# Kernel tuning notes

Measured on AMD Instinct MI355X. Metric: run time of the kernel, lower is better.

## Reference

```python
import jax, jax.numpy as jnp
import numpy as np

I, H = 64, 128


def setup_inputs() -> dict:
    key = jax.random.key(0)
    k1, k2, k3, k4, k5, k6 = jax.random.split(key, 6)
    B, T = 4096, 200
    stdv = 1.0 / np.sqrt(H)
    inp = jax.random.normal(k1, (B, T, I), dtype=jnp.float32)
    seq_lengths = jax.random.randint(k2, (B,), 0, T, dtype=jnp.int32)
    # PyTorch GRUCell params: weight_ih [3H, I], weight_hh [3H, H], biases [3H]; gate order r, z, n
    W_ih = jax.random.uniform(k3, (3 * H, I), minval=-stdv, maxval=stdv, dtype=jnp.float32)
    W_hh = jax.random.uniform(k4, (3 * H, H), minval=-stdv, maxval=stdv, dtype=jnp.float32)
    b_ih = jax.random.uniform(k5, (3 * H,), minval=-stdv, maxval=stdv, dtype=jnp.float32)
    b_hh = jax.random.uniform(k6, (3 * H,), minval=-stdv, maxval=stdv, dtype=jnp.float32)
    return {"input": inp, "seq_lengths": seq_lengths, "W_ih": W_ih, "W_hh": W_hh, "b_ih": b_ih, "b_hh": b_hh}


def _gru_cell(x, h, W_ih, W_hh, b_ih, b_hh):
    gx = x @ W_ih.T + b_ih  # [B, 3H]
    gh = h @ W_hh.T + b_hh  # [B, 3H]
    xr, xz, xn = jnp.split(gx, 3, axis=1)
    hr, hz, hn = jnp.split(gh, 3, axis=1)
    r = jax.nn.sigmoid(xr + hr)
    z = jax.nn.sigmoid(xz + hz)
    n = jnp.tanh(xn + r * hn)
    return (1.0 - z) * n + z * h


def reference(input, seq_lengths, W_ih, W_hh, b_ih, b_hh):
    B, T, _ = input.shape
    h0 = jnp.zeros((B, H), dtype=input.dtype)
    hn0 = jnp.zeros((B, H), dtype=input.dtype)
    xs = (jnp.swapaxes(input, 0, 1), jnp.arange(T))  # [T, B, I], [T]

    def step(carry, xt):
        h, hn = carry
        x_t, t = xt
        h_new = _gru_cell(x_t, h, W_ih, W_hh, b_ih, b_hh)
        mask = (t + 1 <= seq_lengths).astype(input.dtype)[:, None]  # [B, 1]
        hn_new = mask * h_new + (1.0 - mask) * hn
        return (h_new, hn_new), None

    (_, hn_final), _ = jax.lax.scan(step, (h0, hn0), xs)
    return hn_final
```

## Files before the change

### kernel.cpp

```cpp
#include <hip/hip_runtime.h>


#define I_DIM 64
#define H_DIM 128
#define LDSP 200

typedef _Float16 h8 __attribute__((ext_vector_type(8)));
typedef _Float16 h2 __attribute__((ext_vector_type(2)));
typedef float f4 __attribute__((ext_vector_type(4)));
typedef float f2 __attribute__((ext_vector_type(2)));

__device__ __forceinline__ float fast_rcp(float x) {
    return __builtin_amdgcn_rcpf(x);
}
__device__ __forceinline__ float sigmoid_f(float x) {
    return fast_rcp(1.0f + __expf(-x));
}
__device__ __forceinline__ float tanh_f(float x) {
    return 1.0f - 2.0f * fast_rcp(__expf(2.0f * x) + 1.0f);
}

__global__ __launch_bounds__(512, 2)
void gru_seq_kernel(const float* __restrict__ input,
                    const int* __restrict__ seq_lengths,
                    const float* __restrict__ W_ih,
                    const float* __restrict__ W_hh,
                    const float* __restrict__ b_ih,
                    const float* __restrict__ b_hh,
                    float* __restrict__ out,
                    int B, int T) {
    __shared__ __align__(16) _Float16 a_lds[2][16][LDSP];

    const int tid  = threadIdx.x;
    const int lane = tid & 63;
    const int w    = tid >> 6;
    const int base = blockIdx.x * 16;

    const int lrow = lane & 15;
    const int kgrp = lane >> 4;

    int Lq[4];
#pragma unroll
    for (int q = 0; q < 4; ++q) {
        int gr = base + kgrp * 4 + q;
        Lq[q] = (gr < B) ? seq_lengths[gr] : 0;
    }
    int Lmax = 0;
    for (int i = 0; i < 16; ++i) {
        int gr = base + i;
        int L = (gr < B) ? seq_lengths[gr] : 0;
        Lmax = max(Lmax, L);
    }
    if (Lmax > T) Lmax = T;

    const int c0 = w * 16 + lrow;
    const float br  = b_ih[c0] + b_hh[c0];
    const float bz  = b_ih[H_DIM + c0] + b_hh[H_DIM + c0];
    const float bnh = b_hh[2 * H_DIM + c0];
    const float bnx = b_ih[2 * H_DIM + c0];

    h8 bw[18];
#pragma unroll
    for (int gate = 0; gate < 3; ++gate) {
        const int j = gate * H_DIM + w * 16 + lrow;
#pragma unroll
        for (int kt = 0; kt < 6; ++kt) {
            const int kb = kt * 32 + kgrp * 8;
            const float* src = (kt < 4) ? (W_hh + j * H_DIM + kb)
                                        : (W_ih + j * I_DIM + (kb - H_DIM));
            f4 f0 = *(const f4*)(src);
            f4 f1 = *(const f4*)(src + 4);
            h8 v;
            v[0] = (_Float16)f0[0]; v[1] = (_Float16)f0[1];
            v[2] = (_Float16)f0[2]; v[3] = (_Float16)f0[3];
            v[4] = (_Float16)f1[0]; v[5] = (_Float16)f1[1];
            v[6] = (_Float16)f1[2]; v[7] = (_Float16)f1[3];
            bw[gate * 6 + kt] = v;
        }
    }

    {
        int idx = tid * 4;
        int r = idx >> 7, cc = idx & 127;
        *(h2*)&a_lds[0][r][cc]     = h2{0, 0};
        *(h2*)&a_lds[0][r][cc + 2] = h2{0, 0};
    }
    const int xrow = tid >> 5;
    const int xc2  = (tid & 31) * 2;
    const float* xbase = input + (size_t)(base + xrow) * T * I_DIM + xc2;
    const bool xrow_ok = (base + xrow) < B;
    if (Lmax > 0 && xrow_ok) {
        f2 xv = *(const f2*)(xbase);
        h2 hv; hv[0] = (_Float16)xv[0]; hv[1] = (_Float16)xv[1];
        *(h2*)&a_lds[0][xrow][H_DIM + xc2] = hv;
    }
    __syncthreads();

    float hreg[4]  = {0.f, 0.f, 0.f, 0.f};
    float hnreg[4] = {0.f, 0.f, 0.f, 0.f};

    for (int t = 0; t < Lmax; ++t) {
        const int cur = t & 1, nxt = cur ^ 1;

        f2 xn_v = {0.f, 0.f};
        const bool pf = (t + 1 < Lmax) && xrow_ok;
        if (pf) xn_v = *(const f2*)(xbase + (size_t)(t + 1) * I_DIM);

        h8 af[6];
#pragma unroll
        for (int kt = 0; kt < 6; ++kt)
            af[kt] = *(const h8*)&a_lds[cur][lrow][kt * 32 + kgrp * 8];

        f4 ar  = f4{br, br, br, br};
        f4 az  = f4{bz, bz, bz, bz};
        f4 anh = f4{bnh, bnh, bnh, bnh};
        f4 anx = f4{bnx, bnx, bnx, bnx};
#pragma unroll
        for (int kt = 0; kt < 6; ++kt)
            ar = __builtin_amdgcn_mfma_f32_16x16x32_f16(af[kt], bw[0 * 6 + kt], ar, 0, 0, 0);
#pragma unroll
        for (int kt = 0; kt < 6; ++kt)
            az = __builtin_amdgcn_mfma_f32_16x16x32_f16(af[kt], bw[1 * 6 + kt], az, 0, 0, 0);
#pragma unroll
        for (int kt = 0; kt < 4; ++kt)
            anh = __builtin_amdgcn_mfma_f32_16x16x32_f16(af[kt], bw[2 * 6 + kt], anh, 0, 0, 0);
#pragma unroll
        for (int kt = 4; kt < 6; ++kt)
            anx = __builtin_amdgcn_mfma_f32_16x16x32_f16(af[kt], bw[2 * 6 + kt], anx, 0, 0, 0);

#pragma unroll
        for (int q = 0; q < 4; ++q) {
            float r    = sigmoid_f(ar[q]);
            float z    = sigmoid_f(az[q]);
            float n    = tanh_f(anx[q] + r * anh[q]);
            float h    = hreg[q];
            float hnew = n + z * (h - n);
            hreg[q] = hnew;
            if (t < Lq[q]) hnreg[q] = hnew;
        }

#pragma unroll
        for (int q = 0; q < 4; ++q)
            a_lds[nxt][kgrp * 4 + q][w * 16 + lrow] = (_Float16)hreg[q];
        if (pf) {
            h2 hv; hv[0] = (_Float16)xn_v[0]; hv[1] = (_Float16)xn_v[1];
            *(h2*)&a_lds[nxt][xrow][H_DIM + xc2] = hv;
        }
        __syncthreads();
    }

#pragma unroll
    for (int q = 0; q < 4; ++q) {
        int gr = base + kgrp * 4 + q;
        if (gr < B) out[(size_t)gr * H_DIM + w * 16 + lrow] = hnreg[q];
    }
}

extern "C" void kernel_launch(void* const* d_in, const int* in_sizes, int n_in,
                              void* d_out, int out_size, void* d_ws, size_t ws_size,
                              hipStream_t stream) {
    const float* input = (const float*)d_in[0];
    const int*   seq   = (const int*)d_in[1];
    const float* W_ih  = (const float*)d_in[2];
    const float* W_hh  = (const float*)d_in[3];
    const float* b_ih  = (const float*)d_in[4];
    const float* b_hh  = (const float*)d_in[5];
    float* out = (float*)d_out;

    const int B = in_sizes[1];
    const int T = in_sizes[0] / (B * I_DIM);

    const int grid = (B + 15) / 16;
    gru_seq_kernel<<<grid, 512, 0, stream>>>(input, seq, W_ih, W_hh, b_ih, b_hh, out, B, T);
}
```

Measured before the change: 167.5 us.

## Stage input in 8-step chunks and precompute next-step input projection off critical path

```diff
diff --git a/kernel.cpp b/kernel.cpp
--- a/kernel.cpp
+++ b/kernel.cpp
@@ -3,12 +3,13 @@
 
 #define I_DIM 64
 #define H_DIM 128
-#define LDSP 200
+#define CH 8
+#define HP 136
+#define XP 72
 
 typedef _Float16 h8 __attribute__((ext_vector_type(8)));
-typedef _Float16 h2 __attribute__((ext_vector_type(2)));
+typedef _Float16 h4 __attribute__((ext_vector_type(4)));
 typedef float f4 __attribute__((ext_vector_type(4)));
-typedef float f2 __attribute__((ext_vector_type(2)));
 
 __device__ __forceinline__ float fast_rcp(float x) {
     return __builtin_amdgcn_rcpf(x);
@@ -29,7 +30,8 @@
                     const float* __restrict__ b_hh,
                     float* __restrict__ out,
                     int B, int T) {
-    __shared__ __align__(16) _Float16 a_lds[2][16][LDSP];
+    __shared__ __align__(16) _Float16 h_lds[2][16][HP];
+    __shared__ __align__(16) _Float16 x_lds[2][CH][16][XP];
 
     const int tid  = threadIdx.x;
     const int lane = tid & 63;
@@ -62,7 +64,7 @@
     h8 bw[18];
 #pragma unroll
     for (int gate = 0; gate < 3; ++gate) {
-        const int j = gate * H_DIM + w * 16 + lrow;
+        const int j = gate * H_DIM + c0;
 #pragma unroll
         for (int kt = 0; kt < 6; ++kt) {
             const int kb = kt * 32 + kgrp * 8;
@@ -82,19 +84,48 @@
     {
         int idx = tid * 4;
         int r = idx >> 7, cc = idx & 127;
-        *(h2*)&a_lds[0][r][cc]     = h2{0, 0};
-        *(h2*)&a_lds[0][r][cc + 2] = h2{0, 0};
-    }
-    const int xrow = tid >> 5;
-    const int xc2  = (tid & 31) * 2;
-    const float* xbase = input + (size_t)(base + xrow) * T * I_DIM + xc2;
-    const bool xrow_ok = (base + xrow) < B;
-    if (Lmax > 0 && xrow_ok) {
-        f2 xv = *(const f2*)(xbase);
-        h2 hv; hv[0] = (_Float16)xv[0]; hv[1] = (_Float16)xv[1];
-        *(h2*)&a_lds[0][xrow][H_DIM + xc2] = hv;
+        *(h4*)&h_lds[0][r][cc] = h4{0, 0, 0, 0};
+    }
+
+    const int srow = tid >> 5;
+    const int si0  = (tid & 31) >> 4;
+    const int icol = (tid & 15) * 4;
+    const int gxr  = base + srow;
+    const float* xsrc = input + (size_t)gxr * T * I_DIM;
+    const bool xok = (gxr < B);
+
+    if (Lmax > 0) {
+        f4 xv[4];
+#pragma unroll
+        for (int j = 0; j < 4; ++j) {
+            int s = si0 + 2 * j;
+            xv[j] = f4{0.f, 0.f, 0.f, 0.f};
+            if (xok && s < T) xv[j] = *(const f4*)(xsrc + (size_t)s * I_DIM + icol);
+        }
+#pragma unroll
+        for (int j = 0; j < 4; ++j) {
+            int s = si0 + 2 * j;
+            h4 hv;
+            hv[0] = (_Float16)xv[j][0]; hv[1] = (_Float16)xv[j][1];
+            hv[2] = (_Float16)xv[j][2]; hv[3] = (_Float16)xv[j][3];
+            *(h4*)&x_lds[0][s][srow][icol] = hv;
+        }
     }
     __syncthreads();
+
+    f4 arx  = f4{br, br, br, br};
+    f4 azx  = f4{bz, bz, bz, bz};
+    f4 anxx = f4{bnx, bnx, bnx, bnx};
+    if (Lmax > 0) {
+        h8 xg0 = *(const h8*)&x_lds[0][0][lrow][kgrp * 8];
+        h8 xg1 = *(const h8*)&x_lds[0][0][lrow][32 + kgrp * 8];
+        arx  = __builtin_amdgcn_mfma_f32_16x16x32_f16(xg0, bw[0 * 6 + 4], arx, 0, 0, 0);
+        arx  = __builtin_amdgcn_mfma_f32_16x16x32_f16(xg1, bw[0 * 6 + 5], arx, 0, 0, 0);
+        azx  = __builtin_amdgcn_mfma_f32_16x16x32_f16(xg0, bw[1 * 6 + 4], azx, 0, 0, 0);
+        azx  = __builtin_amdgcn_mfma_f32_16x16x32_f16(xg1, bw[1 * 6 + 5], azx, 0, 0, 0);
+        anxx = __builtin_amdgcn_mfma_f32_16x16x32_f16(xg0, bw[2 * 6 + 4], anxx, 0, 0, 0);
+        anxx = __builtin_amdgcn_mfma_f32_16x16x32_f16(xg1, bw[2 * 6 + 5], anxx, 0, 0, 0);
+    }
 
     float hreg[4]  = {0.f, 0.f, 0.f, 0.f};
     float hnreg[4] = {0.f, 0.f, 0.f, 0.f};
@@ -102,37 +133,61 @@
     for (int t = 0; t < Lmax; ++t) {
         const int cur = t & 1, nxt = cur ^ 1;
 
-        f2 xn_v = {0.f, 0.f};
-        const bool pf = (t + 1 < Lmax) && xrow_ok;
-        if (pf) xn_v = *(const f2*)(xbase + (size_t)(t + 1) * I_DIM);
-
-        h8 af[6];
-#pragma unroll
-        for (int kt = 0; kt < 6; ++kt)
-            af[kt] = *(const h8*)&a_lds[cur][lrow][kt * 32 + kgrp * 8];
-
-        f4 ar  = f4{br, br, br, br};
-        f4 az  = f4{bz, bz, bz, bz};
-        f4 anh = f4{bnh, bnh, bnh, bnh};
-        f4 anx = f4{bnx, bnx, bnx, bnx};
-#pragma unroll
-        for (int kt = 0; kt < 6; ++kt)
-            ar = __builtin_amdgcn_mfma_f32_16x16x32_f16(af[kt], bw[0 * 6 + kt], ar, 0, 0, 0);
-#pragma unroll
-        for (int kt = 0; kt < 6; ++kt)
-            az = __builtin_amdgcn_mfma_f32_16x16x32_f16(af[kt], bw[1 * 6 + kt], az, 0, 0, 0);
-#pragma unroll
-        for (int kt = 0; kt < 4; ++kt)
-            anh = __builtin_amdgcn_mfma_f32_16x16x32_f16(af[kt], bw[2 * 6 + kt], anh, 0, 0, 0);
-#pragma unroll
-        for (int kt = 4; kt < 6; ++kt)
-            anx = __builtin_amdgcn_mfma_f32_16x16x32_f16(af[kt], bw[2 * 6 + kt], anx, 0, 0, 0);
+        f4 xv[4];
+        const bool do_stage = ((t & 7) == 0) && (t + CH < Lmax);
+        if (do_stage) {
+            const int t0 = t + CH;
+#pragma unroll
+            for (int j = 0; j < 4; ++j) {
+                int s = si0 + 2 * j;
+                xv[j] = f4{0.f, 0.f, 0.f, 0.f};
+                if (xok && t0 + s < T) xv[j] = *(const f4*)(xsrc + (size_t)(t0 + s) * I_DIM + icol);
+            }
+        }
+
+        h8 af0 = *(const h8*)&h_lds[cur][lrow][0 * 32 + kgrp * 8];
+        h8 af1 = *(const h8*)&h_lds[cur][lrow][1 * 32 + kgrp * 8];
+        h8 af2 = *(const h8*)&h_lds[cur][lrow][2 * 32 + kgrp * 8];
+        h8 af3 = *(const h8*)&h_lds[cur][lrow][3 * 32 + kgrp * 8];
+        const int slot1 = ((t + 1) >> 3) & 1;
+        const int ss1   = (t + 1) & 7;
+        h8 xg0 = *(const h8*)&x_lds[slot1][ss1][lrow][kgrp * 8];
+        h8 xg1 = *(const h8*)&x_lds[slot1][ss1][lrow][32 + kgrp * 8];
+
+        f4 ar   = arx;
+        f4 az   = azx;
+        f4 anxc = anxx;
+        f4 anh  = f4{bnh, bnh, bnh, bnh};
+        __builtin_amdgcn_s_setprio(1);
+        ar  = __builtin_amdgcn_mfma_f32_16x16x32_f16(af0, bw[0 * 6 + 0], ar, 0, 0, 0);
+        ar  = __builtin_amdgcn_mfma_f32_16x16x32_f16(af1, bw[0 * 6 + 1], ar, 0, 0, 0);
+        ar  = __builtin_amdgcn_mfma_f32_16x16x32_f16(af2, bw[0 * 6 + 2], ar, 0, 0, 0);
+        ar  = __builtin_amdgcn_mfma_f32_16x16x32_f16(af3, bw[0 * 6 + 3], ar, 0, 0, 0);
+        az  = __builtin_amdgcn_mfma_f32_16x16x32_f16(af0, bw[1 * 6 + 0], az, 0, 0, 0);
+        az  = __builtin_amdgcn_mfma_f32_16x16x32_f16(af1, bw[1 * 6 + 1], az, 0, 0, 0);
+        az  = __builtin_amdgcn_mfma_f32_16x16x32_f16(af2, bw[1 * 6 + 2], az, 0, 0, 0);
+        az  = __builtin_amdgcn_mfma_f32_16x16x32_f16(af3, bw[1 * 6 + 3], az, 0, 0, 0);
+        anh = __builtin_amdgcn_mfma_f32_16x16x32_f16(af0, bw[2 * 6 + 0], anh, 0, 0, 0);
+        anh = __builtin_amdgcn_mfma_f32_16x16x32_f16(af1, bw[2 * 6 + 1], anh, 0, 0, 0);
+        anh = __builtin_amdgcn_mfma_f32_16x16x32_f16(af2, bw[2 * 6 + 2], anh, 0, 0, 0);
+        anh = __builtin_amdgcn_mfma_f32_16x16x32_f16(af3, bw[2 * 6 + 3], anh, 0, 0, 0);
+        f4 nrx  = f4{br, br, br, br};
+        f4 nzx  = f4{bz, bz, bz, bz};
+        f4 nnx  = f4{bnx, bnx, bnx, bnx};
+        nrx = __builtin_amdgcn_mfma_f32_16x16x32_f16(xg0, bw[0 * 6 + 4], nrx, 0, 0, 0);
+        nrx = __builtin_amdgcn_mfma_f32_16x16x32_f16(xg1, bw[0 * 6 + 5], nrx, 0, 0, 0);
+        nzx = __builtin_amdgcn_mfma_f32_16x16x32_f16(xg0, bw[1 * 6 + 4], nzx, 0, 0, 0);
+        nzx = __builtin_amdgcn_mfma_f32_16x16x32_f16(xg1, bw[1 * 6 + 5], nzx, 0, 0, 0);
+        nnx = __builtin_amdgcn_mfma_f32_16x16x32_f16(xg0, bw[2 * 6 + 4], nnx, 0, 0, 0);
+        nnx = __builtin_amdgcn_mfma_f32_16x16x32_f16(xg1, bw[2 * 6 + 5], nnx, 0, 0, 0);
+        __builtin_amdgcn_s_setprio(0);
+        arx = nrx; azx = nzx; anxx = nnx;
 
 #pragma unroll
         for (int q = 0; q < 4; ++q) {
             float r    = sigmoid_f(ar[q]);
             float z    = sigmoid_f(az[q]);
-            float n    = tanh_f(anx[q] + r * anh[q]);
+            float n    = tanh_f(anxc[q] + r * anh[q]);
             float h    = hreg[q];
             float hnew = n + z * (h - n);
             hreg[q] = hnew;
@@ -141,10 +196,17 @@
 
 #pragma unroll
         for (int q = 0; q < 4; ++q)
-            a_lds[nxt][kgrp * 4 + q][w * 16 + lrow] = (_Float16)hreg[q];
-        if (pf) {
-            h2 hv; hv[0] = (_Float16)xn_v[0]; hv[1] = (_Float16)xn_v[1];
-            *(h2*)&a_lds[nxt][xrow][H_DIM + xc2] = hv;
+            h_lds[nxt][kgrp * 4 + q][c0] = (_Float16)hreg[q];
+        if (do_stage) {
+            const int wslot = ((t >> 3) & 1) ^ 1;
+#pragma unroll
+            for (int j = 0; j < 4; ++j) {
+                int s = si0 + 2 * j;
+                h4 hv;
+                hv[0] = (_Float16)xv[j][0]; hv[1] = (_Float16)xv[j][1];
+                hv[2] = (_Float16)xv[j][2]; hv[3] = (_Float16)xv[j][3];
+                *(h4*)&x_lds[wslot][s][srow][icol] = hv;
+            }
         }
         __syncthreads();
     }
@@ -152,7 +214,7 @@
 #pragma unroll
     for (int q = 0; q < 4; ++q) {
         int gr = base + kgrp * 4 + q;
-        if (gr < B) out[(size_t)gr * H_DIM + w * 16 + lrow] = hnreg[q];
+        if (gr < B) out[(size_t)gr * H_DIM + c0] = hnreg[q];
     }
 }
 
```

New measurement: 158.9 us. 1.05x faster.

## Precompute next-step input projections and stage input chunks across timesteps

Applied to the files above, without the earlier changes.

```diff
diff --git a/kernel.cpp b/kernel.cpp
--- a/kernel.cpp
+++ b/kernel.cpp
@@ -3,22 +3,16 @@
 
 #define I_DIM 64
 #define H_DIM 128
-#define LDSP 200
+#define CH 8
+#define RS 40
 
 typedef _Float16 h8 __attribute__((ext_vector_type(8)));
-typedef _Float16 h2 __attribute__((ext_vector_type(2)));
+typedef _Float16 h4 __attribute__((ext_vector_type(4)));
 typedef float f4 __attribute__((ext_vector_type(4)));
-typedef float f2 __attribute__((ext_vector_type(2)));
-
-__device__ __forceinline__ float fast_rcp(float x) {
-    return __builtin_amdgcn_rcpf(x);
-}
-__device__ __forceinline__ float sigmoid_f(float x) {
-    return fast_rcp(1.0f + __expf(-x));
-}
-__device__ __forceinline__ float tanh_f(float x) {
-    return 1.0f - 2.0f * fast_rcp(__expf(2.0f * x) + 1.0f);
-}
+
+__device__ __forceinline__ float fast_rcp(float x) { return __builtin_amdgcn_rcpf(x); }
+__device__ __forceinline__ float sigmoid_f(float x) { return fast_rcp(1.0f + __expf(-x)); }
+__device__ __forceinline__ float tanh_f(float x) { return 1.0f - 2.0f * fast_rcp(__expf(2.0f * x) + 1.0f); }
 
 __global__ __launch_bounds__(512, 2)
 void gru_seq_kernel(const float* __restrict__ input,
@@ -29,20 +23,24 @@
                     const float* __restrict__ b_hh,
                     float* __restrict__ out,
                     int B, int T) {
-    __shared__ __align__(16) _Float16 a_lds[2][16][LDSP];
+    __shared__ __align__(16) _Float16 h_lds[2][4][16][RS];
+    __shared__ __align__(16) _Float16 x_lds[2][CH][2][16][RS];
 
     const int tid  = threadIdx.x;
     const int lane = tid & 63;
     const int w    = tid >> 6;
     const int base = blockIdx.x * 16;
-
-    const int lrow = lane & 15;
-    const int kgrp = lane >> 4;
+    const int boff = blockIdx.x % 7;
+
+    const int lrow  = lane & 15;
+    const int kgrp  = lane >> 4;
+    const int kgrp8 = kgrp * 8;
+    const int kgrp4 = kgrp * 4;
 
     int Lq[4];
 #pragma unroll
     for (int q = 0; q < 4; ++q) {
-        int gr = base + kgrp * 4 + q;
+        int gr = base + kgrp4 + q;
         Lq[q] = (gr < B) ? seq_lengths[gr] : 0;
     }
     int Lmax = 0;
@@ -62,10 +60,10 @@
     h8 bw[18];
 #pragma unroll
     for (int gate = 0; gate < 3; ++gate) {
-        const int j = gate * H_DIM + w * 16 + lrow;
+        const int j = gate * H_DIM + c0;
 #pragma unroll
         for (int kt = 0; kt < 6; ++kt) {
-            const int kb = kt * 32 + kgrp * 8;
+            const int kb = kt * 32 + kgrp8;
             const float* src = (kt < 4) ? (W_hh + j * H_DIM + kb)
                                         : (W_ih + j * I_DIM + (kb - H_DIM));
             f4 f0 = *(const f4*)(src);
@@ -81,78 +79,148 @@
 
     {
         int idx = tid * 4;
-        int r = idx >> 7, cc = idx & 127;
-        *(h2*)&a_lds[0][r][cc]     = h2{0, 0};
-        *(h2*)&a_lds[0][r][cc + 2] = h2{0, 0};
-    }
-    const int xrow = tid >> 5;
-    const int xc2  = (tid & 31) * 2;
-    const float* xbase = input + (size_t)(base + xrow) * T * I_DIM + xc2;
-    const bool xrow_ok = (base + xrow) < B;
-    if (Lmax > 0 && xrow_ok) {
-        f2 xv = *(const f2*)(xbase);
-        h2 hv; hv[0] = (_Float16)xv[0]; hv[1] = (_Float16)xv[1];
-        *(h2*)&a_lds[0][xrow][H_DIM + xc2] = hv;
+        int sl = idx >> 9, r = (idx >> 5) & 15, cc = idx & 31;
+        *(h4*)&h_lds[0][sl][r][cc] = h4{0, 0, 0, 0};
+    }
+
+    const int srow  = tid >> 5;
+    const int si0   = (tid & 31) >> 4;
+    const int icol  = (tid & 15) * 4;
+    const int xslab = icol >> 5;
+    const int xcol  = icol & 31;
+    const int gxr   = base + srow;
+    const float* xsrc = input + (size_t)gxr * T * I_DIM;
+    const bool xok = (gxr < B);
+
+    if (Lmax > 0) {
+#pragma unroll
+        for (int j = 0; j < 4; ++j) {
+            int s = si0 + 2 * j;
+            f4 xv = f4{0.f, 0.f, 0.f, 0.f};
+            if (xok && s < T) xv = *(const f4*)(xsrc + (size_t)s * I_DIM + icol);
+            h4 hv;
+            hv[0] = (_Float16)xv[0]; hv[1] = (_Float16)xv[1];
+            hv[2] = (_Float16)xv[2]; hv[3] = (_Float16)xv[3];
+            *(h4*)&x_lds[0][s][xslab][srow][xcol] = hv;
+        }
     }
     __syncthreads();
+
+    f4 xar[2], xaz[2], xan[2];
+    xar[0] = f4{br, br, br, br};
+    xaz[0] = f4{bz, bz, bz, bz};
+    xan[0] = f4{bnx, bnx, bnx, bnx};
+    if (Lmax > 0) {
+        h8 xg0 = *(const h8*)&x_lds[0][0][0][lrow][kgrp8];
+        h8 xg1 = *(const h8*)&x_lds[0][0][1][lrow][kgrp8];
+        xar[0] = __builtin_amdgcn_mfma_f32_16x16x32_f16(xg0, bw[4],  xar[0], 0, 0, 0);
+        xar[0] = __builtin_amdgcn_mfma_f32_16x16x32_f16(xg1, bw[5],  xar[0], 0, 0, 0);
+        xaz[0] = __builtin_amdgcn_mfma_f32_16x16x32_f16(xg0, bw[10], xaz[0], 0, 0, 0);
+        xaz[0] = __builtin_amdgcn_mfma_f32_16x16x32_f16(xg1, bw[11], xaz[0], 0, 0, 0);
+        xan[0] = __builtin_amdgcn_mfma_f32_16x16x32_f16(xg0, bw[16], xan[0], 0, 0, 0);
+        xan[0] = __builtin_amdgcn_mfma_f32_16x16x32_f16(xg1, bw[17], xan[0], 0, 0, 0);
+    }
+
+    const int hs = c0 >> 5;
+    const int hc = c0 & 31;
 
     float hreg[4]  = {0.f, 0.f, 0.f, 0.f};
     float hnreg[4] = {0.f, 0.f, 0.f, 0.f};
 
-    for (int t = 0; t < Lmax; ++t) {
-        const int cur = t & 1, nxt = cur ^ 1;
-
-        f2 xn_v = {0.f, 0.f};
-        const bool pf = (t + 1 < Lmax) && xrow_ok;
-        if (pf) xn_v = *(const f2*)(xbase + (size_t)(t + 1) * I_DIM);
-
-        h8 af[6];
-#pragma unroll
-        for (int kt = 0; kt < 6; ++kt)
-            af[kt] = *(const h8*)&a_lds[cur][lrow][kt * 32 + kgrp * 8];
-
-        f4 ar  = f4{br, br, br, br};
-        f4 az  = f4{bz, bz, bz, bz};
-        f4 anh = f4{bnh, bnh, bnh, bnh};
-        f4 anx = f4{bnx, bnx, bnx, bnx};
-#pragma unroll
-        for (int kt = 0; kt < 6; ++kt)
-            ar = __builtin_amdgcn_mfma_f32_16x16x32_f16(af[kt], bw[0 * 6 + kt], ar, 0, 0, 0);
-#pragma unroll
-        for (int kt = 0; kt < 6; ++kt)
-            az = __builtin_amdgcn_mfma_f32_16x16x32_f16(af[kt], bw[1 * 6 + kt], az, 0, 0, 0);
-#pragma unroll
-        for (int kt = 0; kt < 4; ++kt)
-            anh = __builtin_amdgcn_mfma_f32_16x16x32_f16(af[kt], bw[2 * 6 + kt], anh, 0, 0, 0);
-#pragma unroll
-        for (int kt = 4; kt < 6; ++kt)
-            anx = __builtin_amdgcn_mfma_f32_16x16x32_f16(af[kt], bw[2 * 6 + kt], anx, 0, 0, 0);
-
-#pragma unroll
-        for (int q = 0; q < 4; ++q) {
-            float r    = sigmoid_f(ar[q]);
-            float z    = sigmoid_f(az[q]);
-            float n    = tanh_f(anx[q] + r * anh[q]);
-            float h    = hreg[q];
-            float hnew = n + z * (h - n);
-            hreg[q] = hnew;
-            if (t < Lq[q]) hnreg[q] = hnew;
-        }
-
-#pragma unroll
-        for (int q = 0; q < 4; ++q)
-            a_lds[nxt][kgrp * 4 + q][w * 16 + lrow] = (_Float16)hreg[q];
-        if (pf) {
-            h2 hv; hv[0] = (_Float16)xn_v[0]; hv[1] = (_Float16)xn_v[1];
-            *(h2*)&a_lds[nxt][xrow][H_DIM + xc2] = hv;
-        }
-        __syncthreads();
-    }
+#define STEP(P, TC) do {                                                              \
+        const int t_ = (TC);                                                          \
+        f4 xv0, xv1, xv2, xv3;                                                        \
+        const bool do_stage = ((t_ & 7) == boff) && (((t_ >> 3) + 1) * CH < Lmax);    \
+        if (do_stage) {                                                               \
+            const int t0 = ((t_ >> 3) + 1) * CH;                                      \
+            xv0 = xv1 = xv2 = xv3 = f4{0.f, 0.f, 0.f, 0.f};                           \
+            if (xok) {                                                                \
+                int s0 = t0 + si0;                                                    \
+                if (s0     < T) xv0 = *(const f4*)(xsrc + (size_t)(s0    ) * I_DIM + icol); \
+                if (s0 + 2 < T) xv1 = *(const f4*)(xsrc + (size_t)(s0 + 2) * I_DIM + icol); \
+                if (s0 + 4 < T) xv2 = *(const f4*)(xsrc + (size_t)(s0 + 4) * I_DIM + icol); \
+                if (s0 + 6 < T) xv3 = *(const f4*)(xsrc + (size_t)(s0 + 6) * I_DIM + icol); \
+            }                                                                         \
+        }                                                                             \
+        h8 af0 = *(const h8*)&h_lds[P][0][lrow][kgrp8];                               \
+        h8 af1 = *(const h8*)&h_lds[P][1][lrow][kgrp8];                               \
+        h8 af2 = *(const h8*)&h_lds[P][2][lrow][kgrp8];                               \
+        h8 af3 = *(const h8*)&h_lds[P][3][lrow][kgrp8];                               \
+        f4 ar  = xar[P];                                                              \
+        f4 az  = xaz[P];                                                              \
+        f4 axn = xan[P];                                                              \
+        f4 anh = f4{bnh, bnh, bnh, bnh};                                              \
+        __builtin_amdgcn_s_setprio(1);                                                \
+        ar  = __builtin_amdgcn_mfma_f32_16x16x32_f16(af0, bw[0],  ar,  0, 0, 0);      \
+        az  = __builtin_amdgcn_mfma_f32_16x16x32_f16(af0, bw[6],  az,  0, 0, 0);      \
+        anh = __builtin_amdgcn_mfma_f32_16x16x32_f16(af0, bw[12], anh, 0, 0, 0);      \
+        ar  = __builtin_amdgcn_mfma_f32_16x16x32_f16(af1, bw[1],  ar,  0, 0, 0);      \
+        az  = __builtin_amdgcn_mfma_f32_16x16x32_f16(af1, bw[7],  az,  0, 0, 0);      \
+        anh = __builtin_amdgcn_mfma_f32_16x16x32_f16(af1, bw[13], anh, 0, 0, 0);      \
+        ar  = __builtin_amdgcn_mfma_f32_16x16x32_f16(af2, bw[2],  ar,  0, 0, 0);      \
+        az  = __builtin_amdgcn_mfma_f32_16x16x32_f16(af2, bw[8],  az,  0, 0, 0);      \
+        anh = __builtin_amdgcn_mfma_f32_16x16x32_f16(af2, bw[14], anh, 0, 0, 0);      \
+        ar  = __builtin_amdgcn_mfma_f32_16x16x32_f16(af3, bw[3],  ar,  0, 0, 0);      \
+        az  = __builtin_amdgcn_mfma_f32_16x16x32_f16(af3, bw[9],  az,  0, 0, 0);      \
+        anh = __builtin_amdgcn_mfma_f32_16x16x32_f16(af3, bw[15], anh, 0, 0, 0);      \
+        if (t_ + 1 < Lmax) {              \
+            const int sl_ = ((t_ + 1) >> 3) & 1, ss_ = (t_ + 1) & 7;                  \
+            h8 xg0 = *(const h8*)&x_lds[sl_][ss_][0][lrow][kgrp8];                    \
+            h8 xg1 = *(const h8*)&x_lds[sl_][ss_][1][lrow][kgrp8];                    \
+            f4 a0 = f4{br, br, br, br};                                               \
+            f4 a1 = f4{bz, bz, bz, bz};                                               \
+            f4 a2 = f4{bnx, bnx, bnx, bnx};                                           \
+            a0 = __builtin_amdgcn_mfma_f32_16x16x32_f16(xg0, bw[4],  a0, 0, 0, 0);    \
+            a1 = __builtin_amdgcn_mfma_f32_16x16x32_f16(xg0, bw[10], a1, 0, 0, 0);    \
+            a2 = __builtin_amdgcn_mfma_f32_16x16x32_f16(xg0, bw[16], a2, 0, 0, 0);    \
+            a0 = __builtin_amdgcn_mfma_f32_16x16x32_f16(xg1, bw[5],  a0, 0, 0, 0);    \
+            a1 = __builtin_amdgcn_mfma_f32_16x16x32_f16(xg1, bw[11], a1, 0, 0, 0);    \
+            a2 = __builtin_amdgcn_mfma_f32_16x16x32_f16(xg1, bw[17], a2, 0, 0, 0);    \
+            xar[(P) ^ 1] = a0; xaz[(P) ^ 1] = a1; xan[(P) ^ 1] = a2;                  \
+        }                                                                             \
+        __builtin_amdgcn_s_setprio(0);                                                \
+        _Pragma("unroll")                                                             \
+        for (int q = 0; q < 4; ++q) {                                                 \
+            float r    = sigmoid_f(ar[q]);                                            \
+            float z    = sigmoid_f(az[q]);                                            \
+            float n    = tanh_f(axn[q] + r * anh[q]);                                 \
+            float hnew = n + z * (hreg[q] - n);                                       \
+            hreg[q] = hnew;                                                           \
+            if (t_ < Lq[q]) hnreg[q] = hnew;                                          \
+            h_lds[(P) ^ 1][hs][kgrp4 + q][hc] = (_Float16)hnew;                       \
+        }                                                                             \
+        if (do_stage) {                                                               \
+            const int ws_ = ((t_ >> 3) + 1) & 1;                                      \
+            h4 hv;                                                                    \
+            hv[0] = (_Float16)xv0[0]; hv[1] = (_Float16)xv0[1];                       \
+            hv[2] = (_Float16)xv0[2]; hv[3] = (_Float16)xv0[3];                       \
+            *(h4*)&x_lds[ws_][si0][xslab][srow][xcol] = hv;                           \
+            hv[0] = (_Float16)xv1[0]; hv[1] = (_Float16)xv1[1];                       \
+            hv[2] = (_Float16)xv1[2]; hv[3] = (_Float16)xv1[3];                       \
+            *(h4*)&x_lds[ws_][si0 + 2][xslab][srow][xcol] = hv;                       \
+            hv[0] = (_Float16)xv2[0]; hv[1] = (_Float16)xv2[1];                       \
+            hv[2] = (_Float16)xv2[2]; hv[3] = (_Float16)xv2[3];                       \
+            *(h4*)&x_lds[ws_][si0 + 4][xslab][srow][xcol] = hv;                       \
+            hv[0] = (_Float16)xv3[0]; hv[1] = (_Float16)xv3[1];                       \
+            hv[2] = (_Float16)xv3[2]; hv[3] = (_Float16)xv3[3];                       \
+            *(h4*)&x_lds[ws_][si0 + 6][xslab][srow][xcol] = hv;                       \
+        }                                                                             \
+        __syncthreads();                                                              \
+    } while (0)
+
+    int t = 0;
+    for (; t + 1 < Lmax; t += 2) {
+        STEP(0, t);
+        STEP(1, t + 1);
+    }
+    if (t < Lmax) STEP(0, t);
+
+#undef STEP
 
 #pragma unroll
     for (int q = 0; q < 4; ++q) {
-        int gr = base + kgrp * 4 + q;
-        if (gr < B) out[(size_t)gr * H_DIM + w * 16 + lrow] = hnreg[q];
+        int gr = base + kgrp4 + q;
+        if (gr < B) out[(size_t)gr * H_DIM + c0] = hnreg[q];
     }
 }
 
```

Measured after the change: 164.7 us. No clear change (-1.7%).

## Split GRU block into hidden-path and input-projection warp roles

Applied to the files above, without the earlier changes.

```diff
diff --git a/kernel.cpp b/kernel.cpp
--- a/kernel.cpp
+++ b/kernel.cpp
@@ -3,24 +3,22 @@
 
 #define I_DIM 64
 #define H_DIM 128
-#define LDSP 200
+#define RS 40
+#define LOG2E 1.44269504088896f
 
 typedef _Float16 h8 __attribute__((ext_vector_type(8)));
+typedef _Float16 h4 __attribute__((ext_vector_type(4)));
 typedef _Float16 h2 __attribute__((ext_vector_type(2)));
 typedef float f4 __attribute__((ext_vector_type(4)));
-typedef float f2 __attribute__((ext_vector_type(2)));
-
-__device__ __forceinline__ float fast_rcp(float x) {
-    return __builtin_amdgcn_rcpf(x);
-}
-__device__ __forceinline__ float sigmoid_f(float x) {
-    return fast_rcp(1.0f + __expf(-x));
-}
-__device__ __forceinline__ float tanh_f(float x) {
-    return 1.0f - 2.0f * fast_rcp(__expf(2.0f * x) + 1.0f);
-}
-
-__global__ __launch_bounds__(512, 2)
+
+__device__ __forceinline__ float sig2(float xp) {
+    return __builtin_amdgcn_rcpf(1.0f + __builtin_amdgcn_exp2f(-xp));
+}
+__device__ __forceinline__ float tanh2(float ap) {
+    return 1.0f - 2.0f * __builtin_amdgcn_rcpf(__builtin_amdgcn_exp2f(ap) + 1.0f);
+}
+
+__global__ __launch_bounds__(1024)
 void gru_seq_kernel(const float* __restrict__ input,
                     const int* __restrict__ seq_lengths,
                     const float* __restrict__ W_ih,
@@ -29,22 +27,22 @@
                     const float* __restrict__ b_hh,
                     float* __restrict__ out,
                     int B, int T) {
-    __shared__ __align__(16) _Float16 a_lds[2][16][LDSP];
+    __shared__ __align__(16) _Float16 h_lds[2][4][16][RS];
+    __shared__ __align__(16) _Float16 p_lds[2][3][8][64][4];
 
     const int tid  = threadIdx.x;
     const int lane = tid & 63;
     const int w    = tid >> 6;
+    const int role = w >> 3;
+    const int s    = w & 7;
     const int base = blockIdx.x * 16;
 
-    const int lrow = lane & 15;
-    const int kgrp = lane >> 4;
-
-    int Lq[4];
-#pragma unroll
-    for (int q = 0; q < 4; ++q) {
-        int gr = base + kgrp * 4 + q;
-        Lq[q] = (gr < B) ? seq_lengths[gr] : 0;
-    }
+    const int lrow  = lane & 15;
+    const int kgrp  = lane >> 4;
+    const int kgrp8 = kgrp * 8;
+    const int kgrp4 = kgrp * 4;
+    const int c0    = s * 16 + lrow;
+
     int Lmax = 0;
     for (int i = 0; i < 16; ++i) {
         int gr = base + i;
@@ -52,107 +50,197 @@
         Lmax = max(Lmax, L);
     }
     if (Lmax > T) Lmax = T;
-
-    const int c0 = w * 16 + lrow;
-    const float br  = b_ih[c0] + b_hh[c0];
-    const float bz  = b_ih[H_DIM + c0] + b_hh[H_DIM + c0];
-    const float bnh = b_hh[2 * H_DIM + c0];
-    const float bnx = b_ih[2 * H_DIM + c0];
-
-    h8 bw[18];
-#pragma unroll
-    for (int gate = 0; gate < 3; ++gate) {
-        const int j = gate * H_DIM + w * 16 + lrow;
-#pragma unroll
-        for (int kt = 0; kt < 6; ++kt) {
-            const int kb = kt * 32 + kgrp * 8;
-            const float* src = (kt < 4) ? (W_hh + j * H_DIM + kb)
-                                        : (W_ih + j * I_DIM + (kb - H_DIM));
-            f4 f0 = *(const f4*)(src);
-            f4 f1 = *(const f4*)(src + 4);
-            h8 v;
-            v[0] = (_Float16)f0[0]; v[1] = (_Float16)f0[1];
-            v[2] = (_Float16)f0[2]; v[3] = (_Float16)f0[3];
-            v[4] = (_Float16)f1[0]; v[5] = (_Float16)f1[1];
-            v[6] = (_Float16)f1[2]; v[7] = (_Float16)f1[3];
-            bw[gate * 6 + kt] = v;
-        }
-    }
+    int Lq[4];
+#pragma unroll
+    for (int q = 0; q < 4; ++q) {
+        int gr = base + kgrp4 + q;
+        Lq[q] = (gr < B) ? seq_lengths[gr] : 0;
+    }
+
+    float bnh = 0.f, br = 0.f, bz = 0.f, bnx = 0.f;
+    h8 bw[12];
+    if (role == 0) {
+        bnh = b_hh[2 * H_DIM + c0] * (2.f * LOG2E);
+#pragma unroll
+        for (int g = 0; g < 3; ++g) {
+            const float gs = (g == 2) ? (2.f * LOG2E) : LOG2E;
+            const float* wr = W_hh + (size_t)(g * H_DIM + c0) * H_DIM;
+#pragma unroll
+            for (int kt = 0; kt < 4; ++kt) {
+                f4 f0 = *(const f4*)(wr + kt * 32 + kgrp8);
+                f4 f1 = *(const f4*)(wr + kt * 32 + kgrp8 + 4);
+                h8 v;
+                v[0] = (_Float16)(f0[0] * gs); v[1] = (_Float16)(f0[1] * gs);
+                v[2] = (_Float16)(f0[2] * gs); v[3] = (_Float16)(f0[3] * gs);
+                v[4] = (_Float16)(f1[0] * gs); v[5] = (_Float16)(f1[1] * gs);
+                v[6] = (_Float16)(f1[2] * gs); v[7] = (_Float16)(f1[3] * gs);
+                bw[g * 4 + kt] = v;
+            }
+        }
+    } else {
+        br  = (b_ih[c0] + b_hh[c0]) * LOG2E;
+        bz  = (b_ih[H_DIM + c0] + b_hh[H_DIM + c0]) * LOG2E;
+        bnx = b_ih[2 * H_DIM + c0] * (2.f * LOG2E);
+#pragma unroll
+        for (int g = 0; g < 3; ++g) {
+            const float gs = (g == 2) ? (2.f * LOG2E) : LOG2E;
+            const float* wr = W_ih + (size_t)(g * H_DIM + c0) * I_DIM;
+#pragma unroll
+            for (int kx = 0; kx < 2; ++kx) {
+                f4 f0 = *(const f4*)(wr + kx * 32 + kgrp8);
+                f4 f1 = *(const f4*)(wr + kx * 32 + kgrp8 + 4);
+                h8 v;
+                v[0] = (_Float16)(f0[0] * gs); v[1] = (_Float16)(f0[1] * gs);
+                v[2] = (_Float16)(f0[2] * gs); v[3] = (_Float16)(f0[3] * gs);
+                v[4] = (_Float16)(f1[0] * gs); v[5] = (_Float16)(f1[1] * gs);
+                v[6] = (_Float16)(f1[2] * gs); v[7] = (_Float16)(f1[3] * gs);
+                bw[g * 2 + kx] = v;
+            }
+        }
+    }
+
+    const float* xsrc = input + (size_t)(base + lrow) * T * I_DIM;
+    const bool xok = (base + lrow) < B;
 
     {
-        int idx = tid * 4;
-        int r = idx >> 7, cc = idx & 127;
-        *(h2*)&a_lds[0][r][cc]     = h2{0, 0};
-        *(h2*)&a_lds[0][r][cc + 2] = h2{0, 0};
-    }
-    const int xrow = tid >> 5;
-    const int xc2  = (tid & 31) * 2;
-    const float* xbase = input + (size_t)(base + xrow) * T * I_DIM + xc2;
-    const bool xrow_ok = (base + xrow) < B;
-    if (Lmax > 0 && xrow_ok) {
-        f2 xv = *(const f2*)(xbase);
-        h2 hv; hv[0] = (_Float16)xv[0]; hv[1] = (_Float16)xv[1];
-        *(h2*)&a_lds[0][xrow][H_DIM + xc2] = hv;
+        int idx = tid * 2;
+        int sl = idx >> 9, r = (idx >> 5) & 15, cc = idx & 31;
+        *(h2*)&h_lds[0][sl][r][cc] = h2{0, 0};
     }
     __syncthreads();
+
+    if (role == 1 && Lmax > 0) {
+        f4 xa = f4{0.f,0.f,0.f,0.f}, xb = xa, xc = xa, xd = xa;
+        if (xok) {
+            xa = *(const f4*)(xsrc + kgrp8);
+            xb = *(const f4*)(xsrc + kgrp8 + 4);
+            xc = *(const f4*)(xsrc + 32 + kgrp8);
+            xd = *(const f4*)(xsrc + 32 + kgrp8 + 4);
+        }
+        h8 xg0, xg1;
+        xg0[0]=(_Float16)xa[0]; xg0[1]=(_Float16)xa[1]; xg0[2]=(_Float16)xa[2]; xg0[3]=(_Float16)xa[3];
+        xg0[4]=(_Float16)xb[0]; xg0[5]=(_Float16)xb[1]; xg0[6]=(_Float16)xb[2]; xg0[7]=(_Float16)xb[3];
+        xg1[0]=(_Float16)xc[0]; xg1[1]=(_Float16)xc[1]; xg1[2]=(_Float16)xc[2]; xg1[3]=(_Float16)xc[3];
+        xg1[4]=(_Float16)xd[0]; xg1[5]=(_Float16)xd[1]; xg1[6]=(_Float16)xd[2]; xg1[7]=(_Float16)xd[3];
+        f4 a0 = f4{br, br, br, br};
+        f4 a1 = f4{bz, bz, bz, bz};
+        f4 a2 = f4{bnx, bnx, bnx, bnx};
+        a0 = __builtin_amdgcn_mfma_f32_16x16x32_f16(xg0, bw[0], a0, 0, 0, 0);
+        a1 = __builtin_amdgcn_mfma_f32_16x16x32_f16(xg0, bw[2], a1, 0, 0, 0);
+        a2 = __builtin_amdgcn_mfma_f32_16x16x32_f16(xg0, bw[4], a2, 0, 0, 0);
+        a0 = __builtin_amdgcn_mfma_f32_16x16x32_f16(xg1, bw[1], a0, 0, 0, 0);
+        a1 = __builtin_amdgcn_mfma_f32_16x16x32_f16(xg1, bw[3], a1, 0, 0, 0);
+        a2 = __builtin_amdgcn_mfma_f32_16x16x32_f16(xg1, bw[5], a2, 0, 0, 0);
+        h4 p;
+        p[0]=(_Float16)a0[0]; p[1]=(_Float16)a0[1]; p[2]=(_Float16)a0[2]; p[3]=(_Float16)a0[3];
+        *(h4*)&p_lds[0][0][s][lane][0] = p;
+        p[0]=(_Float16)a1[0]; p[1]=(_Float16)a1[1]; p[2]=(_Float16)a1[2]; p[3]=(_Float16)a1[3];
+        *(h4*)&p_lds[0][1][s][lane][0] = p;
+        p[0]=(_Float16)a2[0]; p[1]=(_Float16)a2[1]; p[2]=(_Float16)a2[2]; p[3]=(_Float16)a2[3];
+        *(h4*)&p_lds[0][2][s][lane][0] = p;
+    }
+    __syncthreads();
+
+    const int hs = c0 >> 5;
+    const int hc = c0 & 31;
 
     float hreg[4]  = {0.f, 0.f, 0.f, 0.f};
     float hnreg[4] = {0.f, 0.f, 0.f, 0.f};
 
-    for (int t = 0; t < Lmax; ++t) {
-        const int cur = t & 1, nxt = cur ^ 1;
-
-        f2 xn_v = {0.f, 0.f};
-        const bool pf = (t + 1 < Lmax) && xrow_ok;
-        if (pf) xn_v = *(const f2*)(xbase + (size_t)(t + 1) * I_DIM);
-
-        h8 af[6];
-#pragma unroll
-        for (int kt = 0; kt < 6; ++kt)
-            af[kt] = *(const h8*)&a_lds[cur][lrow][kt * 32 + kgrp * 8];
-
-        f4 ar  = f4{br, br, br, br};
-        f4 az  = f4{bz, bz, bz, bz};
-        f4 anh = f4{bnh, bnh, bnh, bnh};
-        f4 anx = f4{bnx, bnx, bnx, bnx};
-#pragma unroll
-        for (int kt = 0; kt < 6; ++kt)
-            ar = __builtin_amdgcn_mfma_f32_16x16x32_f16(af[kt], bw[0 * 6 + kt], ar, 0, 0, 0);
-#pragma unroll
-        for (int kt = 0; kt < 6; ++kt)
-            az = __builtin_amdgcn_mfma_f32_16x16x32_f16(af[kt], bw[1 * 6 + kt], az, 0, 0, 0);
-#pragma unroll
-        for (int kt = 0; kt < 4; ++kt)
-            anh = __builtin_amdgcn_mfma_f32_16x16x32_f16(af[kt], bw[2 * 6 + kt], anh, 0, 0, 0);
-#pragma unroll
-        for (int kt = 4; kt < 6; ++kt)
-            anx = __builtin_amdgcn_mfma_f32_16x16x32_f16(af[kt], bw[2 * 6 + kt], anx, 0, 0, 0);
-
+#define STEP(P, TC) do {                                                              \
+        const int t_ = (TC);                                                          \
+        if (role == 0) {                                                              \
+            h8 af0 = *(const h8*)&h_lds[P][0][lrow][kgrp8];                           \
+            h8 af1 = *(const h8*)&h_lds[P][1][lrow][kgrp8];                           \
+            h8 af2 = *(const h8*)&h_lds[P][2][lrow][kgrp8];                           \
+            h8 af3 = *(const h8*)&h_lds[P][3][lrow][kgrp8];                           \
+            h4 p0 = *(const h4*)&p_lds[P][0][s][lane][0];                             \
+            h4 p1 = *(const h4*)&p_lds[P][1][s][lane][0];                             \
+            h4 p2 = *(const h4*)&p_lds[P][2][s][lane][0];                             \
+            f4 ar  = f4{(float)p0[0], (float)p0[1], (float)p0[2], (float)p0[3]};      \
+            f4 az  = f4{(float)p1[0], (float)p1[1], (float)p1[2], (float)p1[3]};      \
+            f4 axn = f4{(float)p2[0], (float)p2[1], (float)p2[2], (float)p2[3]};      \
+            f4 anh = f4{bnh, bnh, bnh, bnh};                                          \
+            __builtin_amdgcn_s_setprio(1);                                            \
+            ar  = __builtin_amdgcn_mfma_f32_16x16x32_f16(af0, bw[0],  ar,  0, 0, 0);  \
+            az  = __builtin_amdgcn_mfma_f32_16x16x32_f16(af0, bw[4],  az,  0, 0, 0);  \
+            anh = __builtin_amdgcn_mfma_f32_16x16x32_f16(af0, bw[8],  anh, 0, 0, 0);  \
+            ar  = __builtin_amdgcn_mfma_f32_16x16x32_f16(af1, bw[1],  ar,  0, 0, 0);  \
+            az  = __builtin_amdgcn_mfma_f32_16x16x32_f16(af1, bw[5],  az,  0, 0, 0);  \
+            anh = __builtin_amdgcn_mfma_f32_16x16x32_f16(af1, bw[9],  anh, 0, 0, 0);  \
+            ar  = __builtin_amdgcn_mfma_f32_16x16x32_f16(af2, bw[2],  ar,  0, 0, 0);  \
+            az  = __builtin_amdgcn_mfma_f32_16x16x32_f16(af2, bw[6],  az,  0, 0, 0);  \
+            anh = __builtin_amdgcn_mfma_f32_16x16x32_f16(af2, bw[10], anh, 0, 0, 0);  \
+            ar  = __builtin_amdgcn_mfma_f32_16x16x32_f16(af3, bw[3],  ar,  0, 0, 0);  \
+            az  = __builtin_amdgcn_mfma_f32_16x16x32_f16(af3, bw[7],  az,  0, 0, 0);  \
+            anh = __builtin_amdgcn_mfma_f32_16x16x32_f16(af3, bw[11], anh, 0, 0, 0);  \
+            __builtin_amdgcn_s_setprio(0);                                            \
+            _Pragma("unroll")                                                         \
+            for (int q = 0; q < 4; ++q) {                                             \
+                float r    = sig2(ar[q]);                                             \
+                float z    = sig2(az[q]);                                             \
+                float n    = tanh2(axn[q] + r * anh[q]);                              \
+                float hnew = n + z * (hreg[q] - n);                                   \
+                hreg[q] = hnew;                                                       \
+                if (t_ < Lq[q]) hnreg[q] = hnew;                                      \
+                h_lds[(P) ^ 1][hs][kgrp4 + q][hc] = (_Float16)hnew;                   \
+            }                                                                         \
+        } else if (t_ + 1 < Lmax) {                                                   \
+            const size_t xo = (size_t)(t_ + 1) * I_DIM;                               \
+            f4 xa = f4{0.f,0.f,0.f,0.f}, xb = xa, xc = xa, xd = xa;                   \
+            if (xok) {                                                                \
+                xa = *(const f4*)(xsrc + xo + kgrp8);                                 \
+                xb = *(const f4*)(xsrc + xo + kgrp8 + 4);                             \
+                xc = *(const f4*)(xsrc + xo + 32 + kgrp8);                            \
+                xd = *(const f4*)(xsrc + xo + 32 + kgrp8 + 4);                        \
+            }                                                                         \
+            h8 xg0, xg1;                                                              \
+            xg0[0]=(_Float16)xa[0]; xg0[1]=(_Float16)xa[1];                           \
+            xg0[2]=(_Float16)xa[2]; xg0[3]=(_Float16)xa[3];                           \
+            xg0[4]=(_Float16)xb[0]; xg0[5]=(_Float16)xb[1];                           \
+            xg0[6]=(_Float16)xb[2]; xg0[7]=(_Float16)xb[3];                           \
+            xg1[0]=(_Float16)xc[0]; xg1[1]=(_Float16)xc[1];                           \
+            xg1[2]=(_Float16)xc[2]; xg1[3]=(_Float16)xc[3];                           \
+            xg1[4]=(_Float16)xd[0]; xg1[5]=(_Float16)xd[1];                           \
+            xg1[6]=(_Float16)xd[2]; xg1[7]=(_Float16)xd[3];                           \
+            f4 a0 = f4{br, br, br, br};                                               \
+            f4 a1 = f4{bz, bz, bz, bz};                                               \
+            f4 a2 = f4{bnx, bnx, bnx, bnx};                                           \
+            a0 = __builtin_amdgcn_mfma_f32_16x16x32_f16(xg0, bw[0], a0, 0, 0, 0);     \
+            a1 = __builtin_amdgcn_mfma_f32_16x16x32_f16(xg0, bw[2], a1, 0, 0, 0);     \
+            a2 = __builtin_amdgcn_mfma_f32_16x16x32_f16(xg0, bw[4], a2, 0, 0, 0);     \
+            a0 = __builtin_amdgcn_mfma_f32_16x16x32_f16(xg1, bw[1], a0, 0, 0, 0);     \
+            a1 = __builtin_amdgcn_mfma_f32_16x16x32_f16(xg1, bw[3], a1, 0, 0, 0);     \
+            a2 = __builtin_amdgcn_mfma_f32_16x16x32_f16(xg1, bw[5], a2, 0, 0, 0);     \
+            h4 p;                                                                     \
+            p[0]=(_Float16)a0[0]; p[1]=(_Float16)a0[1];                               \
+            p[2]=(_Float16)a0[2]; p[3]=(_Float16)a0[3];                               \
+            *(h4*)&p_lds[(P) ^ 1][0][s][lane][0] = p;                                 \
+            p[0]=(_Float16)a1[0]; p[1]=(_Float16)a1[1];                               \
+            p[2]=(_Float16)a1[2]; p[3]=(_Float16)a1[3];                               \
+            *(h4*)&p_lds[(P) ^ 1][1][s][lane][0] = p;                                 \
+            p[0]=(_Float16)a2[0]; p[1]=(_Float16)a2[1];                               \
+            p[2]=(_Float16)a2[2]; p[3]=(_Float16)a2[3];                               \
+            *(h4*)&p_lds[(P) ^ 1][2][s][lane][0] = p;                                 \
+        }                                                                             \
+        __syncthreads();                                                              \
+    } while (0)
+
+    int t = 0;
+    for (; t + 1 < Lmax; t += 2) {
+        STEP(0, t);
+        STEP(1, t + 1);
+    }
+    if (t < Lmax) STEP(0, t);
+
+#undef STEP
+
+    if (role == 0) {
 #pragma unroll
         for (int q = 0; q < 4; ++q) {
-            float r    = sigmoid_f(ar[q]);
-            float z    = sigmoid_f(az[q]);
-            float n    = tanh_f(anx[q] + r * anh[q]);
-            float h    = hreg[q];
-            float hnew = n + z * (h - n);
-            hreg[q] = hnew;
-            if (t < Lq[q]) hnreg[q] = hnew;
-        }
-
-#pragma unroll
-        for (int q = 0; q < 4; ++q)
-            a_lds[nxt][kgrp * 4 + q][w * 16 + lrow] = (_Float16)hreg[q];
-        if (pf) {
-            h2 hv; hv[0] = (_Float16)xn_v[0]; hv[1] = (_Float16)xn_v[1];
-            *(h2*)&a_lds[nxt][xrow][H_DIM + xc2] = hv;
-        }
-        __syncthreads();
-    }
-
-#pragma unroll
-    for (int q = 0; q < 4; ++q) {
-        int gr = base + kgrp * 4 + q;
-        if (gr < B) out[(size_t)gr * H_DIM + w * 16 + lrow] = hnreg[q];
+            int gr = base + kgrp4 + q;
+            if (gr < B) out[(size_t)gr * H_DIM + c0] = hnreg[q];
+        }
     }
 }
 
@@ -171,5 +259,5 @@
     const int T = in_sizes[0] / (B * I_DIM);
 
     const int grid = (B + 15) / 16;
-    gru_seq_kernel<<<grid, 512, 0, stream>>>(input, seq, W_ih, W_hh, b_ih, b_hh, out, B, T);
-}
+    gru_seq_kernel<<<grid, 1024, 0, stream>>>(input, seq, W_ih, W_hh, b_ih, b_hh, out, B, T);
+}
```

Result: slower. 290.1 us (+73.2%).
